# Optimization experiments

Measured on AMD Instinct MI355X. Metric: run time of the kernel, lower is better.

The kernel has to match this reference:

```python
import jax, jax.numpy as jnp
import numpy as np

B = 1_048_576
DIM = 64
NCI_TOTAL = 150_000
FMA_TOTAL = 100_000


def setup_inputs() -> dict:
    key = jax.random.key(0)
    k1, k2, k3, k4, k5, k6, k7 = jax.random.split(key, 7)
    return {
        "pos_n": jax.random.randint(k1, (B,), 0, NCI_TOTAL, dtype=jnp.int64) if jax.config.jax_enable_x64 else jax.random.randint(k1, (B,), 0, NCI_TOTAL, dtype=jnp.int32),
        "pos_m": jax.random.randint(k2, (B,), 0, NCI_TOTAL, dtype=jnp.int32),
        "pos_f": jax.random.randint(k3, (B,), 0, FMA_TOTAL, dtype=jnp.int32),
        "nci_emb": jax.random.normal(k4, (NCI_TOTAL, DIM), dtype=jnp.float32),
        "fma_emb": jax.random.normal(k5, (FMA_TOTAL, DIM), dtype=jnp.float32),
        "n2f_mat": jax.random.normal(k6, (DIM, DIM), dtype=jnp.float32) / np.sqrt(DIM),
        "m2f_mat": jax.random.normal(k7, (DIM, DIM), dtype=jnp.float32) / np.sqrt(DIM),
    }


def reference(pos_n, pos_m, pos_f, nci_emb, fma_emb, n2f_mat, m2f_mat):
    # Embedding gathers. In the original, transfer-matrix lookup ids are all
    # zeros, so the single [dim, dim] matrix is shared across the batch.
    n_e = nci_emb[pos_n]  # [B, D]
    m_e = nci_emb[pos_m]  # [B, D]  (note: pos_m also indexes nci table, per source)
    f_e = fma_emb[pos_f]  # [B, D]

    # TransR-style projection: h = M @ e per sample (shared M).
    h_n = jnp.einsum("ij,bj->bi", n2f_mat, n_e)  # [B, D]
    h_m = jnp.einsum("ij,bj->bi", m2f_mat, m_e)  # [B, D]

    # Squared-diff, sum over dim (the reduce_mean over a size-1 axis is a no-op),
    # then sum over batch.
    n2f_loss = jnp.sum(jnp.square(h_n - f_e))
    m2f_loss = jnp.sum(jnp.square(h_m - f_e))
    return n2f_loss + m2f_loss
```

## Files before the change

kernel.cpp:

```cpp
#include <hip/hip_runtime.h>
#include <hip/hip_fp16.h>


typedef _Float16 half8 __attribute__((ext_vector_type(8)));
typedef __fp16  fp16x2 __attribute__((ext_vector_type(2)));
typedef float floatx16 __attribute__((ext_vector_type(16)));

#define NBLOCKS 1024
#define SAMPLES_PER_BLOCK 128
#define NCI_ELEMS 9600000
#define FMA_ELEMS 6400000

__device__ inline half8 cvt8(float4 a, float4 b) {
    union { half8 h; fp16x2 h2[4]; } u;
    u.h2[0] = __builtin_amdgcn_cvt_pkrtz(a.x, a.y);
    u.h2[1] = __builtin_amdgcn_cvt_pkrtz(a.z, a.w);
    u.h2[2] = __builtin_amdgcn_cvt_pkrtz(b.x, b.y);
    u.h2[3] = __builtin_amdgcn_cvt_pkrtz(b.z, b.w);
    return u.h;
}

__device__ inline uint2 pack4(float4 v) {
    union { fp16x2 h2[2]; uint2 u; } p;
    p.h2[0] = __builtin_amdgcn_cvt_pkrtz(v.x, v.y);
    p.h2[1] = __builtin_amdgcn_cvt_pkrtz(v.z, v.w);
    return p.u;
}

__device__ inline uint2 pack8_fp8(float4 a, float4 b) {
    int lo = 0, hi = 0;
    lo = __builtin_amdgcn_cvt_pk_fp8_f32(a.x, a.y, lo, false);
    lo = __builtin_amdgcn_cvt_pk_fp8_f32(a.z, a.w, lo, true);
    hi = __builtin_amdgcn_cvt_pk_fp8_f32(b.x, b.y, hi, false);
    hi = __builtin_amdgcn_cvt_pk_fp8_f32(b.z, b.w, hi, true);
    uint2 r; r.x = (unsigned)lo; r.y = (unsigned)hi; return r;
}

__global__ __launch_bounds__(256) void convert_kernel(
    const float4* __restrict__ nci, const float4* __restrict__ fma,
    uint2* __restrict__ nci8, uint2* __restrict__ fma8)
{
    const int stride = gridDim.x * blockDim.x;
    const int tid = blockIdx.x * blockDim.x + threadIdx.x;
    for (int i = tid; i < NCI_ELEMS / 8; i += stride)
        nci8[i] = pack8_fp8(nci[2 * i], nci[2 * i + 1]);
    for (int i = tid; i < FMA_ELEMS / 8; i += stride)
        fma8[i] = pack8_fp8(fma[2 * i], fma[2 * i + 1]);
}

__global__ __launch_bounds__(256, 4) void ontomap_kernel_q(
    const int* __restrict__ pos_n, const int* __restrict__ pos_m,
    const int* __restrict__ pos_f,
    const unsigned char* __restrict__ nci8, const unsigned char* __restrict__ fma8,
    const float* __restrict__ n2f, const float* __restrict__ m2f,
    float* __restrict__ out, int iters)
{
    const int lane = threadIdx.x & 63;
    const int wave = threadIdx.x >> 6;
    const int l31  = lane & 31;
    const int hi   = lane >> 5;
    const int kbase = hi * 8;

    long Bn[2][4], Bm[2][4];
#pragma unroll
    for (int nt = 0; nt < 2; ++nt) {
#pragma unroll
        for (int t = 0; t < 4; ++t) {
            const float* p = n2f + (nt * 32 + l31) * 64 + t * 16 + kbase;
            uint2 pb = pack8_fp8(*(const float4*)p, *(const float4*)(p + 4));
            Bn[nt][t] = (long)(((unsigned long)pb.y << 32) | pb.x);
            const float* q = m2f + (nt * 32 + l31) * 64 + t * 16 + kbase;
            uint2 qb = pack8_fp8(*(const float4*)q, *(const float4*)(q + 4));
            Bm[nt][t] = (long)(((unsigned long)qb.y << 32) | qb.x);
        }
    }

    long If8[4];
#pragma unroll
    for (int tp = 0; tp < 4; ++tp) {
        const int n = (tp >> 1) * 32 + l31;
        float4 a, b;
#pragma unroll
        for (int j = 0; j < 4; ++j) {
            ((float*)&a)[j] = (tp * 16 + kbase + j     == n) ? -1.0f : 0.0f;
            ((float*)&b)[j] = (tp * 16 + kbase + j + 4 == n) ? -1.0f : 0.0f;
        }
        uint2 ib = pack8_fp8(a, b);
        If8[tp] = (long)(((unsigned long)ib.y << 32) | ib.x);
    }

    float loss = 0.0f;

    int in_, im_, if_;
    {
        int s = blockIdx.x * SAMPLES_PER_BLOCK + wave * 32 + l31;
        in_ = pos_n[s]; im_ = pos_m[s]; if_ = pos_f[s];
    }

#pragma unroll 1
    for (int it = 0; it < iters; ++it) {
        const int in0 = in_, im0 = im_, if0 = if_;
        if (it + 1 < iters) {
            int s = ((it + 1) * NBLOCKS + blockIdx.x) * SAMPLES_PER_BLOCK
                    + wave * 32 + l31;
            in_ = pos_n[s]; im_ = pos_m[s]; if_ = pos_f[s];
        }

        const unsigned char* pn = nci8 + (long)in0 * 64 + kbase;
        const unsigned char* pm = nci8 + (long)im0 * 64 + kbase;
        const unsigned char* pf = fma8 + (long)if0 * 64 + kbase;

        long An[4], Am[4], Ff[4];
#pragma unroll
        for (int t = 0; t < 4; ++t) {
            An[t] = *(const long*)(pn + t * 16);
            Am[t] = *(const long*)(pm + t * 16);
            Ff[t] = *(const long*)(pf + t * 16);
        }

        {
            floatx16 a{};
#pragma unroll
            for (int t = 0; t < 4; ++t)
                a = __builtin_amdgcn_mfma_f32_32x32x16_fp8_fp8(An[t], Bn[0][t], a, 0, 0, 0);
            a = __builtin_amdgcn_mfma_f32_32x32x16_fp8_fp8(Ff[0], If8[0], a, 0, 0, 0);
            a = __builtin_amdgcn_mfma_f32_32x32x16_fp8_fp8(Ff[1], If8[1], a, 0, 0, 0);
#pragma unroll
            for (int r = 0; r < 16; ++r) loss = fmaf(a[r], a[r], loss);
        }
        {
            floatx16 a{};
#pragma unroll
            for (int t = 0; t < 4; ++t)
                a = __builtin_amdgcn_mfma_f32_32x32x16_fp8_fp8(An[t], Bn[1][t], a, 0, 0, 0);
            a = __builtin_amdgcn_mfma_f32_32x32x16_fp8_fp8(Ff[2], If8[2], a, 0, 0, 0);
            a = __builtin_amdgcn_mfma_f32_32x32x16_fp8_fp8(Ff[3], If8[3], a, 0, 0, 0);
#pragma unroll
            for (int r = 0; r < 16; ++r) loss = fmaf(a[r], a[r], loss);
        }
        {
            floatx16 a{};
#pragma unroll
            for (int t = 0; t < 4; ++t)
                a = __builtin_amdgcn_mfma_f32_32x32x16_fp8_fp8(Am[t], Bm[0][t], a, 0, 0, 0);
            a = __builtin_amdgcn_mfma_f32_32x32x16_fp8_fp8(Ff[0], If8[0], a, 0, 0, 0);
            a = __builtin_amdgcn_mfma_f32_32x32x16_fp8_fp8(Ff[1], If8[1], a, 0, 0, 0);
#pragma unroll
            for (int r = 0; r < 16; ++r) loss = fmaf(a[r], a[r], loss);
        }
        {
            floatx16 a{};
#pragma unroll
            for (int t = 0; t < 4; ++t)
                a = __builtin_amdgcn_mfma_f32_32x32x16_fp8_fp8(Am[t], Bm[1][t], a, 0, 0, 0);
            a = __builtin_amdgcn_mfma_f32_32x32x16_fp8_fp8(Ff[2], If8[2], a, 0, 0, 0);
            a = __builtin_amdgcn_mfma_f32_32x32x16_fp8_fp8(Ff[3], If8[3], a, 0, 0, 0);
#pragma unroll
            for (int r = 0; r < 16; ++r) loss = fmaf(a[r], a[r], loss);
        }
    }

#pragma unroll
    for (int o = 32; o > 0; o >>= 1) loss += __shfl_xor(loss, o, 64);
    if (lane == 0) atomicAdd(out, loss);
}

#define ROW_BYTES 144
__global__ __launch_bounds__(256, 2) void ontomap_kernel_f32(
    const int* __restrict__ pos_n, const int* __restrict__ pos_m,
    const int* __restrict__ pos_f,
    const float* __restrict__ nci, const float* __restrict__ fma_emb,
    const float* __restrict__ n2f, const float* __restrict__ m2f,
    float* __restrict__ out, int iters)
{
    __shared__ char lds[4 * 2 * 32 * ROW_BYTES];

    const int lane = threadIdx.x & 63;
    const int wave = threadIdx.x >> 6;
    const int l31  = lane & 31;
    const int hi   = lane >> 5;
    const int kbase = hi * 8;
    const int srow   = lane >> 4;
    const int schunk = lane & 15;

    char* const nbase = lds + wave * (2 * 32 * ROW_BYTES);
    char* const mbase = nbase + 32 * ROW_BYTES;

    half8 Bn[2][4], Bm[2][4];
#pragma unroll
    for (int nt = 0; nt < 2; ++nt) {
#pragma unroll
        for (int t = 0; t < 4; ++t) {
            const float* p = n2f + (nt * 32 + l31) * 64 + t * 16 + kbase;
            Bn[nt][t] = cvt8(*(const float4*)p, *(const float4*)(p + 4));
            const float* q = m2f + (nt * 32 + l31) * 64 + t * 16 + kbase;
            Bm[nt][t] = cvt8(*(const float4*)q, *(const float4*)(q + 4));
        }
    }

    float loss = 0.0f;
    int in_, im_, if_;
    {
        int s = blockIdx.x * SAMPLES_PER_BLOCK + wave * 32 + l31;
        in_ = pos_n[s]; im_ = pos_m[s]; if_ = pos_f[s];
    }

#pragma unroll 1
    for (int it = 0; it < iters; ++it) {
        const int in0 = in_, im0 = im_, if0 = if_;
        if (it + 1 < iters) {
            int s = ((it + 1) * NBLOCKS + blockIdx.x) * SAMPLES_PER_BLOCK
                    + wave * 32 + l31;
            in_ = pos_n[s]; im_ = pos_m[s]; if_ = pos_f[s];
        }

#pragma unroll
        for (int i = 0; i < 8; ++i) {
            const int rl = i * 4 + srow;
            const int rn = __shfl(in0, rl, 64);
            float4 v = ((const float4*)(nci + (long)rn * 64))[schunk];
            *(uint2*)(nbase + rl * ROW_BYTES + schunk * 8) = pack4(v);
            const int rm = __shfl(im0, rl, 64);
            float4 w = ((const float4*)(nci + (long)rm * 64))[schunk];
            *(uint2*)(mbase + rl * ROW_BYTES + schunk * 8) = pack4(w);
        }
        asm volatile("" ::: "memory");

        floatx16 aN0{}, aN1{}, aM0{}, aM1{};
#pragma unroll
        for (int t = 0; t < 4; ++t) {
            half8 aF = *(const half8*)(nbase + l31 * ROW_BYTES + t * 32 + hi * 16);
            aN0 = __builtin_amdgcn_mfma_f32_32x32x16_f16(aF, Bn[0][t], aN0, 0, 0, 0);
            aN1 = __builtin_amdgcn_mfma_f32_32x32x16_f16(aF, Bn[1][t], aN1, 0, 0, 0);
            half8 bF = *(const half8*)(mbase + l31 * ROW_BYTES + t * 32 + hi * 16);
            aM0 = __builtin_amdgcn_mfma_f32_32x32x16_f16(bF, Bm[0][t], aM0, 0, 0, 0);
            aM1 = __builtin_amdgcn_mfma_f32_32x32x16_f16(bF, Bm[1][t], aM1, 0, 0, 0);
        }

#pragma unroll
        for (int r = 0; r < 16; ++r) {
            const int mrow = (r & 3) + 8 * (r >> 2) + 4 * hi;
            const int fid  = __shfl(if0, mrow, 64);
            const float* pf = fma_emb + (long)fid * 64 + l31;
            const float f0 = pf[0];
            const float f1 = pf[32];
            float d;
            d = aN0[r] - f0; loss = fmaf(d, d, loss);
            d = aM0[r] - f0; loss = fmaf(d, d, loss);
            d = aN1[r] - f1; loss = fmaf(d, d, loss);
            d = aM1[r] - f1; loss = fmaf(d, d, loss);
        }
    }

#pragma unroll
    for (int o = 32; o > 0; o >>= 1) loss += __shfl_xor(loss, o, 64);
    if (lane == 0) atomicAdd(out, loss);
}

extern "C" void kernel_launch(void* const* d_in, const int* in_sizes, int n_in,
                              void* d_out, int out_size, void* d_ws, size_t ws_size,
                              hipStream_t stream) {
    const int*   pos_n   = (const int*)d_in[0];
    const int*   pos_m   = (const int*)d_in[1];
    const int*   pos_f   = (const int*)d_in[2];
    const float* nci_emb = (const float*)d_in[3];
    const float* fma_emb = (const float*)d_in[4];
    const float* n2f_mat = (const float*)d_in[5];
    const float* m2f_mat = (const float*)d_in[6];
    float* out = (float*)d_out;

    const int B = in_sizes[0];
    const int iters = B / (NBLOCKS * SAMPLES_PER_BLOCK);

    (void)hipMemsetAsync(out, 0, sizeof(float), stream);

    const size_t need = (size_t)NCI_ELEMS + (size_t)FMA_ELEMS;
    if (ws_size >= need) {
        unsigned char* nci8 = (unsigned char*)d_ws;
        unsigned char* fma8 = nci8 + NCI_ELEMS;
        convert_kernel<<<2048, 256, 0, stream>>>(
            (const float4*)nci_emb, (const float4*)fma_emb,
            (uint2*)nci8, (uint2*)fma8);
        ontomap_kernel_q<<<NBLOCKS, 256, 0, stream>>>(
            pos_n, pos_m, pos_f, nci8, fma8, n2f_mat, m2f_mat, out, iters);
    } else {
        ontomap_kernel_f32<<<NBLOCKS, 256, 0, stream>>>(
            pos_n, pos_m, pos_f, nci_emb, fma_emb, n2f_mat, m2f_mat, out, iters);
    }
}
```

Baseline: 193.2 us.

## Double-buffer fp8 row gathers and use contiguous 16-byte loads per lane

```diff
diff --git a/kernel.cpp b/kernel.cpp
--- a/kernel.cpp
+++ b/kernel.cpp
@@ -7,7 +7,7 @@
 typedef float floatx16 __attribute__((ext_vector_type(16)));
 
 #define NBLOCKS 1024
-#define SAMPLES_PER_BLOCK 128
+#define SPB 128
 #define NCI_ELEMS 9600000
 #define FMA_ELEMS 6400000
 
@@ -36,6 +36,11 @@
     uint2 r; r.x = (unsigned)lo; r.y = (unsigned)hi; return r;
 }
 
+__device__ inline long pack8_fp8_l(const float* p) {
+    uint2 b = pack8_fp8(*(const float4*)p, *(const float4*)(p + 4));
+    return (long)(((unsigned long)b.y << 32) | b.x);
+}
+
 __global__ __launch_bounds__(256) void convert_kernel(
     const float4* __restrict__ nci, const float4* __restrict__ fma,
     uint2* __restrict__ nci8, uint2* __restrict__ fma8)
@@ -48,7 +53,77 @@
         fma8[i] = pack8_fp8(fma[2 * i], fma[2 * i + 1]);
 }
 
-__global__ __launch_bounds__(256, 4) void ontomap_kernel_q(
+struct FragSet { ulonglong2 n0, n1, m0, m1, f0, f1; };
+
+__device__ inline FragSet gather_frags(
+    const unsigned char* __restrict__ nci8, const unsigned char* __restrict__ fma8,
+    int in0, int im0, int if0, int hoff)
+{
+    FragSet s;
+    const unsigned char* pn = nci8 + (long)in0 * 64 + hoff;
+    const unsigned char* pm = nci8 + (long)im0 * 64 + hoff;
+    const unsigned char* pf = fma8 + (long)if0 * 64 + hoff;
+    s.n0 = *(const ulonglong2*)pn;  s.n1 = *(const ulonglong2*)(pn + 16);
+    s.m0 = *(const ulonglong2*)pm;  s.m1 = *(const ulonglong2*)(pm + 16);
+    s.f0 = *(const ulonglong2*)pf;  s.f1 = *(const ulonglong2*)(pf + 16);
+    return s;
+}
+
+__device__ inline void compute_set(
+    const FragSet& s, const long Bn[2][4], const long Bm[2][4],
+    const long If0[4], const long If1[4], float& loss)
+{
+    const long An[4] = {(long)s.n0.x, (long)s.n0.y, (long)s.n1.x, (long)s.n1.y};
+    const long Am[4] = {(long)s.m0.x, (long)s.m0.y, (long)s.m1.x, (long)s.m1.y};
+    const long Ff[4] = {(long)s.f0.x, (long)s.f0.y, (long)s.f1.x, (long)s.f1.y};
+
+    {
+        floatx16 a{};
+#pragma unroll
+        for (int t = 0; t < 4; ++t)
+            a = __builtin_amdgcn_mfma_f32_32x32x16_fp8_fp8(An[t], Bn[0][t], a, 0, 0, 0);
+#pragma unroll
+        for (int t = 0; t < 4; ++t)
+            a = __builtin_amdgcn_mfma_f32_32x32x16_fp8_fp8(Ff[t], If0[t], a, 0, 0, 0);
+#pragma unroll
+        for (int r = 0; r < 16; ++r) loss = fmaf(a[r], a[r], loss);
+    }
+    {
+        floatx16 a{};
+#pragma unroll
+        for (int t = 0; t < 4; ++t)
+            a = __builtin_amdgcn_mfma_f32_32x32x16_fp8_fp8(An[t], Bn[1][t], a, 0, 0, 0);
+#pragma unroll
+        for (int t = 0; t < 4; ++t)
+            a = __builtin_amdgcn_mfma_f32_32x32x16_fp8_fp8(Ff[t], If1[t], a, 0, 0, 0);
+#pragma unroll
+        for (int r = 0; r < 16; ++r) loss = fmaf(a[r], a[r], loss);
+    }
+    {
+        floatx16 a{};
+#pragma unroll
+        for (int t = 0; t < 4; ++t)
+            a = __builtin_amdgcn_mfma_f32_32x32x16_fp8_fp8(Am[t], Bm[0][t], a, 0, 0, 0);
+#pragma unroll
+        for (int t = 0; t < 4; ++t)
+            a = __builtin_amdgcn_mfma_f32_32x32x16_fp8_fp8(Ff[t], If0[t], a, 0, 0, 0);
+#pragma unroll
+        for (int r = 0; r < 16; ++r) loss = fmaf(a[r], a[r], loss);
+    }
+    {
+        floatx16 a{};
+#pragma unroll
+        for (int t = 0; t < 4; ++t)
+            a = __builtin_amdgcn_mfma_f32_32x32x16_fp8_fp8(Am[t], Bm[1][t], a, 0, 0, 0);
+#pragma unroll
+        for (int t = 0; t < 4; ++t)
+            a = __builtin_amdgcn_mfma_f32_32x32x16_fp8_fp8(Ff[t], If1[t], a, 0, 0, 0);
+#pragma unroll
+        for (int r = 0; r < 16; ++r) loss = fmaf(a[r], a[r], loss);
+    }
+}
+
+__global__ __launch_bounds__(256, 3) void ontomap_kernel_q(
     const int* __restrict__ pos_n, const int* __restrict__ pos_m,
     const int* __restrict__ pos_f,
     const unsigned char* __restrict__ nci8, const unsigned char* __restrict__ fma8,
@@ -59,105 +134,49 @@
     const int wave = threadIdx.x >> 6;
     const int l31  = lane & 31;
     const int hi   = lane >> 5;
-    const int kbase = hi * 8;
+    const int hoff = hi * 32;
 
     long Bn[2][4], Bm[2][4];
 #pragma unroll
     for (int nt = 0; nt < 2; ++nt) {
 #pragma unroll
         for (int t = 0; t < 4; ++t) {
-            const float* p = n2f + (nt * 32 + l31) * 64 + t * 16 + kbase;
-            uint2 pb = pack8_fp8(*(const float4*)p, *(const float4*)(p + 4));
-            Bn[nt][t] = (long)(((unsigned long)pb.y << 32) | pb.x);
-            const float* q = m2f + (nt * 32 + l31) * 64 + t * 16 + kbase;
-            uint2 qb = pack8_fp8(*(const float4*)q, *(const float4*)(q + 4));
-            Bm[nt][t] = (long)(((unsigned long)qb.y << 32) | qb.x);
-        }
-    }
-
-    long If8[4];
-#pragma unroll
-    for (int tp = 0; tp < 4; ++tp) {
-        const int n = (tp >> 1) * 32 + l31;
-        float4 a, b;
-#pragma unroll
-        for (int j = 0; j < 4; ++j) {
-            ((float*)&a)[j] = (tp * 16 + kbase + j     == n) ? -1.0f : 0.0f;
-            ((float*)&b)[j] = (tp * 16 + kbase + j + 4 == n) ? -1.0f : 0.0f;
-        }
-        uint2 ib = pack8_fp8(a, b);
-        If8[tp] = (long)(((unsigned long)ib.y << 32) | ib.x);
-    }
+            Bn[nt][t] = pack8_fp8_l(n2f + (nt * 32 + l31) * 64 + hoff + t * 8);
+            Bm[nt][t] = pack8_fp8_l(m2f + (nt * 32 + l31) * 64 + hoff + t * 8);
+        }
+    }
+
+    long If0[4], If1[4];
+#pragma unroll
+    for (int t = 0; t < 4; ++t) {
+        const unsigned j = (unsigned)(l31 - t * 8);
+        const long pat = (j < 8) ? (long)(0xB8ULL << (8 * j)) : 0L;
+        If0[t] = hi ? 0L : pat;
+        If1[t] = hi ? pat : 0L;
+    }
+
+    const int base = blockIdx.x * SPB + wave * 32 + l31;
+    const int istep = NBLOCKS * SPB;
+
+    int aN = pos_n[base], aM = pos_m[base], aF = pos_f[base];
+    int bN = 0, bM = 0, bF = 0;
+    if (1 < iters) { bN = pos_n[istep + base]; bM = pos_m[istep + base]; bF = pos_f[istep + base]; }
+    FragSet F0 = gather_frags(nci8, fma8, aN, aM, aF, hoff);
+    FragSet F1 = gather_frags(nci8, fma8, bN, bM, bF, hoff);
+    int cN = 0, cM = 0, cF = 0;
+    if (2 < iters) { int s = 2 * istep + base; cN = pos_n[s]; cM = pos_m[s]; cF = pos_f[s]; }
 
     float loss = 0.0f;
 
-    int in_, im_, if_;
-    {
-        int s = blockIdx.x * SAMPLES_PER_BLOCK + wave * 32 + l31;
-        in_ = pos_n[s]; im_ = pos_m[s]; if_ = pos_f[s];
-    }
-
 #pragma unroll 1
-    for (int it = 0; it < iters; ++it) {
-        const int in0 = in_, im0 = im_, if0 = if_;
-        if (it + 1 < iters) {
-            int s = ((it + 1) * NBLOCKS + blockIdx.x) * SAMPLES_PER_BLOCK
-                    + wave * 32 + l31;
-            in_ = pos_n[s]; im_ = pos_m[s]; if_ = pos_f[s];
-        }
-
-        const unsigned char* pn = nci8 + (long)in0 * 64 + kbase;
-        const unsigned char* pm = nci8 + (long)im0 * 64 + kbase;
-        const unsigned char* pf = fma8 + (long)if0 * 64 + kbase;
-
-        long An[4], Am[4], Ff[4];
-#pragma unroll
-        for (int t = 0; t < 4; ++t) {
-            An[t] = *(const long*)(pn + t * 16);
-            Am[t] = *(const long*)(pm + t * 16);
-            Ff[t] = *(const long*)(pf + t * 16);
-        }
-
-        {
-            floatx16 a{};
-#pragma unroll
-            for (int t = 0; t < 4; ++t)
-                a = __builtin_amdgcn_mfma_f32_32x32x16_fp8_fp8(An[t], Bn[0][t], a, 0, 0, 0);
-            a = __builtin_amdgcn_mfma_f32_32x32x16_fp8_fp8(Ff[0], If8[0], a, 0, 0, 0);
-            a = __builtin_amdgcn_mfma_f32_32x32x16_fp8_fp8(Ff[1], If8[1], a, 0, 0, 0);
-#pragma unroll
-            for (int r = 0; r < 16; ++r) loss = fmaf(a[r], a[r], loss);
-        }
-        {
-            floatx16 a{};
-#pragma unroll
-            for (int t = 0; t < 4; ++t)
-                a = __builtin_amdgcn_mfma_f32_32x32x16_fp8_fp8(An[t], Bn[1][t], a, 0, 0, 0);
-            a = __builtin_amdgcn_mfma_f32_32x32x16_fp8_fp8(Ff[2], If8[2], a, 0, 0, 0);
-            a = __builtin_amdgcn_mfma_f32_32x32x16_fp8_fp8(Ff[3], If8[3], a, 0, 0, 0);
-#pragma unroll
-            for (int r = 0; r < 16; ++r) loss = fmaf(a[r], a[r], loss);
-        }
-        {
-            floatx16 a{};
-#pragma unroll
-            for (int t = 0; t < 4; ++t)
-                a = __builtin_amdgcn_mfma_f32_32x32x16_fp8_fp8(Am[t], Bm[0][t], a, 0, 0, 0);
-            a = __builtin_amdgcn_mfma_f32_32x32x16_fp8_fp8(Ff[0], If8[0], a, 0, 0, 0);
-            a = __builtin_amdgcn_mfma_f32_32x32x16_fp8_fp8(Ff[1], If8[1], a, 0, 0, 0);
-#pragma unroll
-            for (int r = 0; r < 16; ++r) loss = fmaf(a[r], a[r], loss);
-        }
-        {
-            floatx16 a{};
-#pragma unroll
-            for (int t = 0; t < 4; ++t)
-                a = __builtin_amdgcn_mfma_f32_32x32x16_fp8_fp8(Am[t], Bm[1][t], a, 0, 0, 0);
-            a = __builtin_amdgcn_mfma_f32_32x32x16_fp8_fp8(Ff[2], If8[2], a, 0, 0, 0);
-            a = __builtin_amdgcn_mfma_f32_32x32x16_fp8_fp8(Ff[3], If8[3], a, 0, 0, 0);
-#pragma unroll
-            for (int r = 0; r < 16; ++r) loss = fmaf(a[r], a[r], loss);
-        }
+    for (int it = 0; it < iters; it += 2) {
+        compute_set(F0, Bn, Bm, If0, If1, loss);
+        if (it + 2 < iters) F0 = gather_frags(nci8, fma8, cN, cM, cF, hoff);
+        int dN = 0, dM = 0, dF = 0;
+        if (it + 3 < iters) { int s = (it + 3) * istep + base; dN = pos_n[s]; dM = pos_m[s]; dF = pos_f[s]; }
+        compute_set(F1, Bn, Bm, If0, If1, loss);
+        if (it + 3 < iters) F1 = gather_frags(nci8, fma8, dN, dM, dF, hoff);
+        if (it + 4 < iters) { int s = (it + 4) * istep + base; cN = pos_n[s]; cM = pos_m[s]; cF = pos_f[s]; }
     }
 
 #pragma unroll
@@ -201,7 +220,7 @@
     float loss = 0.0f;
     int in_, im_, if_;
     {
-        int s = blockIdx.x * SAMPLES_PER_BLOCK + wave * 32 + l31;
+        int s = blockIdx.x * SPB + wave * 32 + l31;
         in_ = pos_n[s]; im_ = pos_m[s]; if_ = pos_f[s];
     }
 
@@ -209,8 +228,7 @@
     for (int it = 0; it < iters; ++it) {
         const int in0 = in_, im0 = im_, if0 = if_;
         if (it + 1 < iters) {
-            int s = ((it + 1) * NBLOCKS + blockIdx.x) * SAMPLES_PER_BLOCK
-                    + wave * 32 + l31;
+            int s = ((it + 1) * NBLOCKS + blockIdx.x) * SPB + wave * 32 + l31;
             in_ = pos_n[s]; im_ = pos_m[s]; if_ = pos_f[s];
         }
 
@@ -270,7 +288,7 @@
     float* out = (float*)d_out;
 
     const int B = in_sizes[0];
-    const int iters = B / (NBLOCKS * SAMPLES_PER_BLOCK);
+    const int iters = B / (NBLOCKS * SPB);
 
     (void)hipMemsetAsync(out, 0, sizeof(float), stream);
 
```

Result: slower. 307.4 us (+59.1%).
